# Kernel tuning notes

Hardware: AMD Instinct MI355X
Metric: run time of the kernel (lower is better)

## Reference

```python
import jax, jax.numpy as jnp
import numpy as np

N = 200000      # tweet nodes
E = 1600000     # edges
U = 20000       # users (num_users)
D = 64          # embedding_dimension1 == embedding_dimension2
NUMP, CATP = 20, 12
EPS = 0.1       # PyG FAConv default eps


def setup_inputs() -> dict:
    key = jax.random.key(0)
    ks = jax.random.split(key, 20)
    s = 0.05
    offs = jnp.sort(jax.random.randint(ks[3], (U + 1,), 0, N, dtype=jnp.int64))
    offs = offs.at[0].set(0).at[-1].set(N)
    return {
        "num_prop": jax.random.normal(ks[0], (N, NUMP), jnp.float32),
        "cat_prop": jax.random.normal(ks[1], (N, CATP), jnp.float32),
        "tweet_offsets": offs,
        "edge_index": jax.random.randint(ks[2], (2, E), 0, N, dtype=jnp.int64),
        "re_index": jax.random.randint(ks[4], (U,), 0, U, dtype=jnp.int64),
        "W_num": jax.random.normal(ks[5], (NUMP, D // 2), jnp.float32) * s,
        "b_num": jnp.zeros((D // 2,), jnp.float32),
        "W_cat": jax.random.normal(ks[6], (CATP, D // 2), jnp.float32) * s,
        "b_cat": jnp.zeros((D // 2,), jnp.float32),
        "W_tog": jax.random.normal(ks[7], (D, D), jnp.float32) * s,
        "b_tog": jnp.zeros((D,), jnp.float32),
        "att_l": jax.random.normal(ks[8], (D,), jnp.float32) * s,
        "att_r": jax.random.normal(ks[9], (D,), jnp.float32) * s,
        "W_f1": jax.random.normal(ks[10], (D, D // 2), jnp.float32) * s,
        "b_f1": jnp.zeros((D // 2,), jnp.float32),
        "W_lab": jax.random.normal(ks[11], (D // 2, 2), jnp.float32) * s,
        "b_lab": jnp.zeros((2,), jnp.float32),
    }


def reference(num_prop, cat_prop, tweet_offsets, edge_index, re_index,
              W_num, b_num, W_cat, b_cat, W_tog, b_tog,
              att_l, att_r, W_f1, b_f1, W_lab, b_lab):
    n = num_prop.shape[0]
    lrelu = jax.nn.leaky_relu  # slope 0.01, matches nn.LeakyReLU default

    num = lrelu(num_prop @ W_num + b_num)
    cat = lrelu(cat_prop @ W_cat + b_cat)
    x = lrelu(jnp.concatenate([num, cat], axis=1) @ W_tog + b_tog)  # [N, D]

    # gcn_norm with self-loops (PyG FAConv default normalize=True, add_self_loops=True)
    loop = jnp.arange(n, dtype=edge_index.dtype)
    src = jnp.concatenate([edge_index[0], loop])
    dst = jnp.concatenate([edge_index[1], loop])
    deg = jax.ops.segment_sum(jnp.ones(src.shape[0], jnp.float32), dst, num_segments=n)
    dinv = jnp.where(deg > 0, deg ** -0.5, 0.0)
    norm = dinv[src] * dinv[dst]  # [E+N]

    def faconv(h, h0):
        # alpha_e = tanh(att_l . h[src] + att_r . h[dst]); out_i = sum_e norm_e * alpha_e * h[src_e]
        al = h @ att_l
        ar = h @ att_r
        alpha = jnp.tanh(al[src] + ar[dst]) * norm
        agg = jax.ops.segment_sum(h[src] * alpha[:, None], dst, num_segments=n)
        return agg + EPS * h0

    x1 = faconv(x, x)      # dropout is identity in eval mode
    x2 = faconv(x1, x)
    x2 = jnp.sqrt(x2 ** 2 + 1e-8)

    # ragged per-user segment sum from CSR offsets (replaces python loop+slice)
    nseg = tweet_offsets.shape[0] - 1
    seg = jnp.searchsorted(tweet_offsets, jnp.arange(n), side='right') - 1
    seg = jnp.clip(seg, 0, nseg - 1)
    x3 = jax.ops.segment_sum(x2, seg, num_segments=nseg)  # [U, D]

    x3 = x3[re_index]
    h = lrelu(x3 @ W_f1 + b_f1)
    return h @ W_lab + b_lab
```

## Files before the change

kernel.cpp:

```cpp
#include <hip/hip_runtime.h>
#include <hip/hip_bf16.h>

#define LRELU(v) ((v) > 0.0f ? (v) : 0.01f * (v))
#define EPS 0.1f

#define BSHIFT  9
#define BSIZE   512
#define BIN_EPB 2048
#define BIN_CAP 6144
#define CAPP    10240

typedef __attribute__((ext_vector_type(8))) short bf16x8;
typedef __attribute__((ext_vector_type(4))) float f32x4;

__device__ __forceinline__ float fast_tanh(float v)
{
    float e = __expf(2.0f * v);
    return 1.0f - 2.0f * __builtin_amdgcn_rcpf(e + 1.0f);
}

__device__ __forceinline__ float bf2f(unsigned short h)
{
    return __uint_as_float(((unsigned int)h) << 16);
}
__device__ __forceinline__ unsigned short f2bf(float f)
{
    unsigned int u = __float_as_uint(f);
    u += 0x7FFFu + ((u >> 16) & 1u);
    return (unsigned short)(u >> 16);
}

__global__ void k_prep(const float* __restrict__ W_num, const float* __restrict__ W_cat,
                       const float* __restrict__ W_tog,
                       unsigned short* __restrict__ Wb, unsigned short* __restrict__ Wb1)
{
    int t = threadIdx.x;
    for (int i = t; i < 8 * 512; i += 256) {
        int tile = i >> 9;
        int kt   = tile >> 2, nt = tile & 3;
        int lane = (i >> 3) & 63;
        int j    = i & 7;
        int k    = kt * 32 + (lane >> 4) * 8 + j;
        int n    = nt * 16 + (lane & 15);
        Wb[i] = f2bf(W_tog[k * 64 + n]);
    }
    for (int i = t; i < 4 * 512; i += 256) {
        int nt   = i >> 9;
        int lane = (i >> 3) & 63;
        int j    = i & 7;
        int k    = (lane >> 4) * 8 + j;
        int n    = nt * 16 + (lane & 15);
        float w;
        if (n < 32) w = (k < 20)  ? W_num[k * 32 + n]              : 0.0f;
        else        w = (k >= 20) ? W_cat[(k - 20) * 32 + (n - 32)] : 0.0f;
        Wb1[i] = f2bf(w);
    }
}

__global__ void __launch_bounds__(512)
k_featbin(
          const float* __restrict__ num_prop, const float* __restrict__ cat_prop,
          const unsigned short* __restrict__ Wb1, const float* __restrict__ b_num,
          const float* __restrict__ b_cat, const unsigned short* __restrict__ Wb,
          const float* __restrict__ b_tog, const float* __restrict__ att_l,
          const float* __restrict__ att_r, unsigned short* __restrict__ xb,
          float* __restrict__ al, float* __restrict__ ar,
          const int* __restrict__ src, const int* __restrict__ dst,
          int* __restrict__ bucket_cnt, int* __restrict__ buckets,
          int nbBin, int N, int E, int NB)
{
    __shared__ __align__(16) char shmem[28672];

    int tid = threadIdx.x;

    if ((int)blockIdx.x < nbBin) {
        int*  hist  = (int*)shmem;
        int*  lbase = hist + BSIZE;
        int*  gbase = lbase + BSIZE;
        int2* stage = (int2*)(gbase + BSIZE);

        int base = blockIdx.x * BIN_EPB;

        hist[tid] = 0;
        __syncthreads();

        int s[4], d[4], rk[4];
        #pragma unroll
        for (int k = 0; k < 4; k++) {
            int e = base + k * BSIZE + tid;
            s[k] = -1;
            if (e < E) {
                s[k] = src[e];
                d[k] = dst[e];
                rk[k] = atomicAdd(&hist[d[k] >> BSHIFT], 1);
            }
        }
        __syncthreads();

        int v = hist[tid];
        lbase[tid] = v;
        __syncthreads();
        for (int off = 1; off < BSIZE; off <<= 1) {
            int t = (tid >= off) ? lbase[tid - off] : 0;
            __syncthreads();
            lbase[tid] += t;
            __syncthreads();
        }
        int incl = lbase[tid];
        __syncthreads();
        lbase[tid] = incl - v;
        if (tid < NB && v > 0) gbase[tid] = atomicAdd(&bucket_cnt[tid], v);
        __syncthreads();

        #pragma unroll
        for (int k = 0; k < 4; k++) {
            if (s[k] >= 0) {
                int b = d[k] >> BSHIFT;
                stage[lbase[b] + rk[k]] = make_int2(s[k], d[k]);
            }
        }
        __syncthreads();

        int tot = min(BIN_EPB, E - base);
        for (int i = tid; i < tot; i += BSIZE) {
            int2 p = stage[i];
            int b = p.y >> BSHIFT;
            buckets[(size_t)b * BIN_CAP + gbase[b] + (i - lbase[b])] =
                (p.x << BSHIFT) | (p.y & (BSIZE - 1));
        }
    } else {
        unsigned short (*in_lds)[40] = (unsigned short(*)[40])shmem;
        unsigned short (*mid)[72]    = (unsigned short(*)[72])(shmem + 10240);

        int lane = tid & 63;
        int w    = tid >> 6;
        int blockStart = (blockIdx.x - nbBin) * 128;

        for (int i = tid; i < 128 * 20; i += 512) {
            int node = i / 20, k = i % 20;
            int n = min(blockStart + node, N - 1);
            in_lds[node][k] = f2bf(num_prop[(size_t)n * 20 + k]);
        }
        for (int i = tid; i < 128 * 12; i += 512) {
            int node = i / 12, k = i % 12;
            int n = min(blockStart + node, N - 1);
            in_lds[node][20 + k] = f2bf(cat_prop[(size_t)n * 12 + k]);
        }
        __syncthreads();

        int q   = lane >> 4;
        int c16 = lane & 15;

        bf16x8 ain = *(const bf16x8*)&in_lds[w * 16 + c16][q * 8];
        #pragma unroll
        for (int nt = 0; nt < 4; nt++) {
            bf16x8 b = *(const bf16x8*)&Wb1[nt * 512 + lane * 8];
            f32x4 acc = {0.0f, 0.0f, 0.0f, 0.0f};
            acc = __builtin_amdgcn_mfma_f32_16x16x32_bf16(ain, b, acc, 0, 0, 0);
            int   ch   = nt * 16 + c16;
            float bias = (ch < 32) ? b_num[ch] : b_cat[ch - 32];
            #pragma unroll
            for (int r = 0; r < 4; r++) {
                float s = acc[r] + bias;
                s = LRELU(s);
                mid[w * 16 + q * 4 + r][ch] = f2bf(s);
            }
        }

        bf16x8 a0 = *(const bf16x8*)&mid[w * 16 + c16][q * 8];
        bf16x8 a1 = *(const bf16x8*)&mid[w * 16 + c16][32 + q * 8];

        float pal[4] = {0, 0, 0, 0};
        float par[4] = {0, 0, 0, 0};

        #pragma unroll
        for (int nt = 0; nt < 4; nt++) {
            bf16x8 b0 = *(const bf16x8*)&Wb[(0 * 4 + nt) * 512 + lane * 8];
            bf16x8 b1 = *(const bf16x8*)&Wb[(1 * 4 + nt) * 512 + lane * 8];
            f32x4 acc = {0.0f, 0.0f, 0.0f, 0.0f};
            acc = __builtin_amdgcn_mfma_f32_16x16x32_bf16(a0, b0, acc, 0, 0, 0);
            acc = __builtin_amdgcn_mfma_f32_16x16x32_bf16(a1, b1, acc, 0, 0, 0);

            int   ch  = nt * 16 + c16;
            float bt  = b_tog[ch];
            float atl = att_l[ch];
            float atr = att_r[ch];
            #pragma unroll
            for (int r = 0; r < 4; r++) {
                float s = acc[r] + bt;
                s = LRELU(s);
                int n = blockStart + w * 16 + q * 4 + r;
                if (n < N) xb[(size_t)n * 64 + ch] = f2bf(s);
                pal[r] = fmaf(s, atl, pal[r]);
                par[r] = fmaf(s, atr, par[r]);
            }
        }

        #pragma unroll
        for (int r = 0; r < 4; r++) {
            float pl = pal[r], pr = par[r];
            #pragma unroll
            for (int off = 8; off > 0; off >>= 1) {
                pl += __shfl_xor(pl, off);
                pr += __shfl_xor(pr, off);
            }
            int n = blockStart + w * 16 + q * 4 + r;
            if (c16 == 0 && n < N) { al[n] = pl; ar[n] = pr; }
        }
    }
}

__global__ void __launch_bounds__(512)
k_build(const int* __restrict__ buckets, const int* __restrict__ bucket_cnt,
        const float* __restrict__ al, const int* __restrict__ offs,
        float2* __restrict__ ald1,
        int* __restrict__ deg, int* __restrict__ row_start, int* __restrict__ seg,
        int* __restrict__ srcs, int N, int U)
{
    __shared__ int stage[BIN_CAP];
    __shared__ int cnt[BSIZE];
    __shared__ int sc[BSIZE];
    __shared__ int cur[BSIZE];

    int b   = blockIdx.x;
    int tid = threadIdx.x;
    int ecnt = bucket_cnt[b];
    const int* bp = buckets + (size_t)b * BIN_CAP;

    cnt[tid] = 0;
    cur[tid] = 0;
    __syncthreads();

    for (int i = tid; i < ecnt; i += BSIZE) {
        int e = bp[i];
        stage[i] = e;
        atomicAdd(&cnt[e & (BSIZE - 1)], 1);
    }
    __syncthreads();

    int d = cnt[tid];
    int p = (d + 7) & ~7;
    sc[tid] = p;
    __syncthreads();
    for (int off = 1; off < BSIZE; off <<= 1) {
        int t = (tid >= off) ? sc[tid - off] : 0;
        __syncthreads();
        sc[tid] += t;
        __syncthreads();
    }
    int rstart = sc[tid] - p;

    int gb = b * CAPP;
    int n  = b * BSIZE + tid;
    if (n < N) {
        deg[n]       = d;
        row_start[n] = gb + rstart;
        for (int k = d; k < p; k++) srcs[gb + rstart + k] = 0;
        float dv = 1.0f / sqrtf((float)d + 1.0f);
        ald1[n] = make_float2(al[n], dv);

        int lo = 0, hi = U;
        while (lo < hi) {
            int mid = (lo + hi) >> 1;
            if (offs[mid] <= n) lo = mid + 1; else hi = mid;
        }
        seg[n] = min(max(lo - 1, 0), U - 1);
    }
    __syncthreads();

    for (int i = tid; i < ecnt; i += BSIZE) {
        int e = stage[i];
        int r = e & (BSIZE - 1);
        int o = atomicAdd(&cur[r], 1);
        int rs = sc[r] - ((cnt[r] + 7) & ~7);
        srcs[gb + rs + o] = e >> BSHIFT;
    }
}

__global__ void k_gather1(const int* __restrict__ srcs,
                          const int* __restrict__ row_start, const int* __restrict__ deg,
                          const unsigned short* __restrict__ xb,
                          const float2* __restrict__ ald1, const float* __restrict__ ar,
                          const float* __restrict__ att_l, const float* __restrict__ att_r,
                          unsigned short* __restrict__ h1b, float2* __restrict__ ald2,
                          float* __restrict__ ar2, int N)
{
    int lane = threadIdx.x & 63;
    int c0   = __builtin_amdgcn_readfirstlane(blockIdx.x * 4 + (threadIdx.x >> 6)) * 4;
    if (c0 >= N) return;
    int nend = min(c0 + 4, N);

    float atl = att_l[lane];
    float atr = att_r[lane];

    for (int n = c0; n < nend; n++) {
        int    s0   = row_start[n];
        int    cnt  = deg[n];
        int    cntp = (cnt + 7) & ~7;
        float2 self = ald1[n];
        float  di   = self.y;
        float  arn  = ar[n];

        float acc = 0.0f;
        for (int jb = 0; jb < cntp; jb += 64) {
            float a = 0.0f;
            int   e = jb + lane;
            if (e < cnt) {
                int s = srcs[s0 + e];
                float2 as = ald1[s];
                a = fast_tanh(as.x + arn) * as.y * di;
            }
            int te = min(cntp - jb, 64);
            for (int j = 0; j < te; j += 8) {
                int sv[8]; float vv[8];
                #pragma unroll
                for (int t = 0; t < 8; t++) sv[t] = srcs[s0 + jb + j + t];
                #pragma unroll
                for (int t = 0; t < 8; t++) vv[t] = bf2f(xb[(size_t)sv[t] * 64 + lane]);
                #pragma unroll
                for (int t = 0; t < 8; t++) acc = fmaf(vv[t], __shfl(a, j + t), acc);
            }
        }

        float selfa = fast_tanh(self.x + arn) * di * di;
        float xnl   = bf2f(xb[(size_t)n * 64 + lane]);
        float v     = acc + (selfa + EPS) * xnl;

        float pl = v * atl;
        float pr = v * atr;
        #pragma unroll
        for (int off = 32; off > 0; off >>= 1) {
            pl += __shfl_down(pl, off);
            pr += __shfl_down(pr, off);
        }
        h1b[(size_t)n * 64 + lane] = f2bf(v);
        if (lane == 0) { ald2[n] = make_float2(pl, di); ar2[n] = pr; }
    }
}

__global__ void k_gather2(const int* __restrict__ srcs,
                          const int* __restrict__ row_start, const int* __restrict__ deg,
                          const unsigned short* __restrict__ h1b,
                          const unsigned short* __restrict__ xb,
                          const float2* __restrict__ ald2, const float* __restrict__ ar2,
                          const int* __restrict__ seg,
                          float* __restrict__ x3, int N)
{
    int lane = threadIdx.x & 63;
    int c0   = __builtin_amdgcn_readfirstlane(blockIdx.x * 4 + (threadIdx.x >> 6)) * 4;
    if (c0 >= N) return;
    int nend = min(c0 + 4, N);

    float uacc = 0.0f;
    int   useg = seg[c0];

    for (int n = c0; n < nend; n++) {
        int sg = seg[n];
        if (sg != useg) {
            atomicAdd(&x3[(size_t)useg * 64 + lane], uacc);
            uacc = 0.0f;
            useg = sg;
        }

        int    s0   = row_start[n];
        int    cnt  = deg[n];
        int    cntp = (cnt + 7) & ~7;
        float2 self = ald2[n];
        float  di   = self.y;
        float  arn  = ar2[n];

        float acc = 0.0f;
        for (int jb = 0; jb < cntp; jb += 64) {
            float a = 0.0f;
            int   e = jb + lane;
            if (e < cnt) {
                int s = srcs[s0 + e];
                float2 as = ald2[s];
                a = fast_tanh(as.x + arn) * as.y * di;
            }
            int te = min(cntp - jb, 64);
            for (int j = 0; j < te; j += 8) {
                int sv[8]; float vv[8];
                #pragma unroll
                for (int t = 0; t < 8; t++) sv[t] = srcs[s0 + jb + j + t];
                #pragma unroll
                for (int t = 0; t < 8; t++) vv[t] = bf2f(h1b[(size_t)sv[t] * 64 + lane]);
                #pragma unroll
                for (int t = 0; t < 8; t++) acc = fmaf(vv[t], __shfl(a, j + t), acc);
            }
        }

        float selfa = fast_tanh(self.x + arn) * di * di;
        float h1l   = bf2f(h1b[(size_t)n * 64 + lane]);
        float xnl   = bf2f(xb[(size_t)n * 64 + lane]);
        float v = acc + selfa * h1l + EPS * xnl;
        uacc += sqrtf(v * v + 1e-8f);
    }
    atomicAdd(&x3[(size_t)useg * 64 + lane], uacc);
}

__global__ void __launch_bounds__(256)
k_head(const float* __restrict__ x3, const int* __restrict__ re_index,
       const float* __restrict__ W_f1, const float* __restrict__ b_f1,
       const float* __restrict__ W_lab, const float* __restrict__ b_lab,
       float* __restrict__ out, int U)
{
    __shared__ float wf[64][32];
    __shared__ float wl[32][2];

    int tid = threadIdx.x;
    for (int i = tid; i < 64 * 32; i += 256) wf[i >> 5][i & 31] = W_f1[i];
    if (tid < 64) wl[tid >> 1][tid & 1] = W_lab[tid];
    __syncthreads();

    int u = blockIdx.x * blockDim.x + tid;
    if (u >= U) return;

    int r = re_index[u];
    const float* y = x3 + (size_t)r * 64;

    float s[32];
    #pragma unroll
    for (int j = 0; j < 32; j++) s[j] = b_f1[j];

    for (int k = 0; k < 64; k++) {
        float yk = y[k];
        #pragma unroll
        for (int j = 0; j < 32; j++) s[j] = fmaf(yk, wf[k][j], s[j]);
    }

    float o0 = b_lab[0], o1 = b_lab[1];
    #pragma unroll
    for (int j = 0; j < 32; j++) {
        float t = LRELU(s[j]);
        o0 = fmaf(t, wl[j][0], o0);
        o1 = fmaf(t, wl[j][1], o1);
    }
    out[(size_t)u * 2 + 0] = o0;
    out[(size_t)u * 2 + 1] = o1;
}

extern "C" void kernel_launch(void* const* d_in, const int* in_sizes, int n_in,
                              void* d_out, int out_size, void* d_ws, size_t ws_size,
                              hipStream_t stream)
{
    const float* num_prop = (const float*)d_in[0];
    const float* cat_prop = (const float*)d_in[1];
    const int*   offs     = (const int*)d_in[2];
    const int*   edge     = (const int*)d_in[3];
    const int*   re_index = (const int*)d_in[4];
    const float* W_num    = (const float*)d_in[5];
    const float* b_num    = (const float*)d_in[6];
    const float* W_cat    = (const float*)d_in[7];
    const float* b_cat    = (const float*)d_in[8];
    const float* W_tog    = (const float*)d_in[9];
    const float* b_tog    = (const float*)d_in[10];
    const float* att_l    = (const float*)d_in[11];
    const float* att_r    = (const float*)d_in[12];
    const float* W_f1     = (const float*)d_in[13];
    const float* b_f1     = (const float*)d_in[14];
    const float* W_lab    = (const float*)d_in[15];
    const float* b_lab    = (const float*)d_in[16];

    const int N = in_sizes[0] / 20;
    const int E = in_sizes[3] / 2;
    const int U = in_sizes[4];

    const int* src = edge;
    const int* dst = edge + E;

    const int NB = (N + BSIZE - 1) >> BSHIFT;

    float* ws = (float*)d_ws;
    size_t off = 0;
    unsigned short* xb  = (unsigned short*)(ws + off); off += (size_t)N * 32;
    unsigned short* h1b = (unsigned short*)(ws + off); off += (size_t)N * 32;
    float2* ald1 = (float2*)(ws + off); off += (size_t)N * 2;
    float2* ald2 = (float2*)(ws + off); off += (size_t)N * 2;
    int*    buckets = (int*)(ws + off); off += (size_t)NB * BIN_CAP;
    float*  al   = ws + off; off += N;
    float*  ar   = ws + off; off += N;
    float*  ar2  = ws + off; off += N;
    float*  x3   = ws + off; off += (size_t)U * 64;
    unsigned short* Wb  = (unsigned short*)(ws + off); off += 2048;
    unsigned short* Wb1 = (unsigned short*)(ws + off); off += 1024;
    int*    deg        = (int*)(ws + off); off += N;
    int*    row_start  = (int*)(ws + off); off += N;
    int*    seg        = (int*)(ws + off); off += N;
    int*    bucket_cnt = (int*)(ws + off); off += NB;
    int*    srcs       = (int*)(ws + off); off += (size_t)NB * CAPP;

    hipMemsetAsync(bucket_cnt, 0, (size_t)NB * 4, stream);
    hipMemsetAsync(x3, 0, (size_t)U * 64 * 4, stream);

    const int nbC    = (N + 15) / 16;
    const int nbBin  = (E + BIN_EPB - 1) / BIN_EPB;
    const int nbFeat = (N + 127) / 128;

    k_prep<<<1, 256, 0, stream>>>(W_num, W_cat, W_tog, Wb, Wb1);

    k_featbin<<<nbBin + nbFeat, 512, 0, stream>>>(num_prop, cat_prop, Wb1, b_num,
                                                  b_cat, Wb, b_tog, att_l, att_r,
                                                  xb, al, ar,
                                                  src, dst, bucket_cnt, buckets,
                                                  nbBin, N, E, NB);

    k_build<<<NB, BSIZE, 0, stream>>>(buckets, bucket_cnt, al, offs, ald1,
                                      deg, row_start, seg, srcs, N, U);

    k_gather1<<<nbC, 256, 0, stream>>>(srcs, row_start, deg, xb, ald1, ar,
                                       att_l, att_r, h1b, ald2, ar2, N);

    k_gather2<<<nbC, 256, 0, stream>>>(srcs, row_start, deg, h1b, xb,
                                       ald2, ar2, seg, x3, N);

    k_head<<<(U + 255) / 256, 256, 0, stream>>>(x3, re_index, W_f1, b_f1, W_lab, b_lab,
                                                (float*)d_out, U);
}
```

Before: 324.2 us.

## Pack per-node metadata, fold memsets into kernels, and double nodes per wave

Per-node row start and degree are packed into one int2, and al/dinv/ar into one float4 (likewise for the second layer), so each node's metadata needs fewer separate loads. The two hipMemsetAsync calls are removed: bucket counters are now zeroed in k_prep and the x3 accumulator in k_build, which cuts launch overhead. Each wave in both gather kernels now handles 8 nodes instead of 4, halving the grid and allowing longer per-user accumulation runs before the atomic flush. The trade-offs are fewer waves available to hide gather latency and a larger 16-byte record in the random per-edge source lookups, which may waste bandwidth.

```diff
diff --git a/kernel.cpp b/kernel.cpp
--- a/kernel.cpp
+++ b/kernel.cpp
@@ -9,6 +9,7 @@
 #define BIN_EPB 2048
 #define BIN_CAP 6144
 #define CAPP    10240
+#define CHUNK   8
 
 typedef __attribute__((ext_vector_type(8))) short bf16x8;
 typedef __attribute__((ext_vector_type(4))) float f32x4;
@@ -32,9 +33,11 @@
 
 __global__ void k_prep(const float* __restrict__ W_num, const float* __restrict__ W_cat,
                        const float* __restrict__ W_tog,
-                       unsigned short* __restrict__ Wb, unsigned short* __restrict__ Wb1)
+                       unsigned short* __restrict__ Wb, unsigned short* __restrict__ Wb1,
+                       int* __restrict__ bucket_cnt, int NB)
 {
     int t = threadIdx.x;
+    for (int i = t; i < NB; i += 256) bucket_cnt[i] = 0;
     for (int i = t; i < 8 * 512; i += 256) {
         int tile = i >> 9;
         int kt   = tile >> 2, nt = tile & 3;
@@ -212,10 +215,11 @@
 
 __global__ void __launch_bounds__(512)
 k_build(const int* __restrict__ buckets, const int* __restrict__ bucket_cnt,
-        const float* __restrict__ al, const int* __restrict__ offs,
-        float2* __restrict__ ald1,
-        int* __restrict__ deg, int* __restrict__ row_start, int* __restrict__ seg,
-        int* __restrict__ srcs, int N, int U)
+        const float* __restrict__ al, const float* __restrict__ ar,
+        const int* __restrict__ offs,
+        float4* __restrict__ aldr1,
+        int2* __restrict__ rd, int* __restrict__ seg,
+        int* __restrict__ srcs, float* __restrict__ x3, int N, int U)
 {
     __shared__ int stage[BIN_CAP];
     __shared__ int cnt[BSIZE];
@@ -226,6 +230,10 @@
     int tid = threadIdx.x;
     int ecnt = bucket_cnt[b];
     const int* bp = buckets + (size_t)b * BIN_CAP;
+
+    size_t u64 = (size_t)U * 64;
+    for (size_t i = (size_t)b * BSIZE + tid; i < u64; i += (size_t)gridDim.x * BSIZE)
+        x3[i] = 0.0f;
 
     cnt[tid] = 0;
     cur[tid] = 0;
@@ -253,11 +261,10 @@
     int gb = b * CAPP;
     int n  = b * BSIZE + tid;
     if (n < N) {
-        deg[n]       = d;
-        row_start[n] = gb + rstart;
+        rd[n] = make_int2(gb + rstart, d);
         for (int k = d; k < p; k++) srcs[gb + rstart + k] = 0;
         float dv = 1.0f / sqrtf((float)d + 1.0f);
-        ald1[n] = make_float2(al[n], dv);
+        aldr1[n] = make_float4(al[n], dv, ar[n], 0.0f);
 
         int lo = 0, hi = U;
         while (lo < hi) {
@@ -278,28 +285,29 @@
 }
 
 __global__ void k_gather1(const int* __restrict__ srcs,
-                          const int* __restrict__ row_start, const int* __restrict__ deg,
+                          const int2* __restrict__ rd,
                           const unsigned short* __restrict__ xb,
-                          const float2* __restrict__ ald1, const float* __restrict__ ar,
+                          const float4* __restrict__ aldr1,
                           const float* __restrict__ att_l, const float* __restrict__ att_r,
-                          unsigned short* __restrict__ h1b, float2* __restrict__ ald2,
-                          float* __restrict__ ar2, int N)
+                          unsigned short* __restrict__ h1b, float4* __restrict__ aldr2,
+                          int N)
 {
     int lane = threadIdx.x & 63;
-    int c0   = __builtin_amdgcn_readfirstlane(blockIdx.x * 4 + (threadIdx.x >> 6)) * 4;
+    int c0   = __builtin_amdgcn_readfirstlane(blockIdx.x * 4 + (threadIdx.x >> 6)) * CHUNK;
     if (c0 >= N) return;
-    int nend = min(c0 + 4, N);
+    int nend = min(c0 + CHUNK, N);
 
     float atl = att_l[lane];
     float atr = att_r[lane];
 
     for (int n = c0; n < nend; n++) {
-        int    s0   = row_start[n];
-        int    cnt  = deg[n];
+        int2   rdn  = rd[n];
+        int    s0   = rdn.x;
+        int    cnt  = rdn.y;
         int    cntp = (cnt + 7) & ~7;
-        float2 self = ald1[n];
+        float4 self = aldr1[n];
         float  di   = self.y;
-        float  arn  = ar[n];
+        float  arn  = self.z;
 
         float acc = 0.0f;
         for (int jb = 0; jb < cntp; jb += 64) {
@@ -307,7 +315,7 @@
             int   e = jb + lane;
             if (e < cnt) {
                 int s = srcs[s0 + e];
-                float2 as = ald1[s];
+                float2 as = *(const float2*)&aldr1[s];
                 a = fast_tanh(as.x + arn) * as.y * di;
             }
             int te = min(cntp - jb, 64);
@@ -334,22 +342,22 @@
             pr += __shfl_down(pr, off);
         }
         h1b[(size_t)n * 64 + lane] = f2bf(v);
-        if (lane == 0) { ald2[n] = make_float2(pl, di); ar2[n] = pr; }
+        if (lane == 0) aldr2[n] = make_float4(pl, di, pr, 0.0f);
     }
 }
 
 __global__ void k_gather2(const int* __restrict__ srcs,
-                          const int* __restrict__ row_start, const int* __restrict__ deg,
+                          const int2* __restrict__ rd,
                           const unsigned short* __restrict__ h1b,
                           const unsigned short* __restrict__ xb,
-                          const float2* __restrict__ ald2, const float* __restrict__ ar2,
+                          const float4* __restrict__ aldr2,
                           const int* __restrict__ seg,
                           float* __restrict__ x3, int N)
 {
     int lane = threadIdx.x & 63;
-    int c0   = __builtin_amdgcn_readfirstlane(blockIdx.x * 4 + (threadIdx.x >> 6)) * 4;
+    int c0   = __builtin_amdgcn_readfirstlane(blockIdx.x * 4 + (threadIdx.x >> 6)) * CHUNK;
     if (c0 >= N) return;
-    int nend = min(c0 + 4, N);
+    int nend = min(c0 + CHUNK, N);
 
     float uacc = 0.0f;
     int   useg = seg[c0];
@@ -362,12 +370,13 @@
             useg = sg;
         }
 
-        int    s0   = row_start[n];
-        int    cnt  = deg[n];
+        int2   rdn  = rd[n];
+        int    s0   = rdn.x;
+        int    cnt  = rdn.y;
         int    cntp = (cnt + 7) & ~7;
-        float2 self = ald2[n];
+        float4 self = aldr2[n];
         float  di   = self.y;
-        float  arn  = ar2[n];
+        float  arn  = self.z;
 
         float acc = 0.0f;
         for (int jb = 0; jb < cntp; jb += 64) {
@@ -375,7 +384,7 @@
             int   e = jb + lane;
             if (e < cnt) {
                 int s = srcs[s0 + e];
-                float2 as = ald2[s];
+                float2 as = *(const float2*)&aldr2[s];
                 a = fast_tanh(as.x + arn) * as.y * di;
             }
             int te = min(cntp - jb, 64);
@@ -473,31 +482,26 @@
 
     float* ws = (float*)d_ws;
     size_t off = 0;
+    float4* aldr1 = (float4*)(ws + off); off += (size_t)N * 4;
+    float4* aldr2 = (float4*)(ws + off); off += (size_t)N * 4;
     unsigned short* xb  = (unsigned short*)(ws + off); off += (size_t)N * 32;
     unsigned short* h1b = (unsigned short*)(ws + off); off += (size_t)N * 32;
-    float2* ald1 = (float2*)(ws + off); off += (size_t)N * 2;
-    float2* ald2 = (float2*)(ws + off); off += (size_t)N * 2;
     int*    buckets = (int*)(ws + off); off += (size_t)NB * BIN_CAP;
     float*  al   = ws + off; off += N;
     float*  ar   = ws + off; off += N;
-    float*  ar2  = ws + off; off += N;
     float*  x3   = ws + off; off += (size_t)U * 64;
     unsigned short* Wb  = (unsigned short*)(ws + off); off += 2048;
     unsigned short* Wb1 = (unsigned short*)(ws + off); off += 1024;
-    int*    deg        = (int*)(ws + off); off += N;
-    int*    row_start  = (int*)(ws + off); off += N;
+    int2*   rd         = (int2*)(ws + off); off += (size_t)N * 2;
     int*    seg        = (int*)(ws + off); off += N;
     int*    bucket_cnt = (int*)(ws + off); off += NB;
     int*    srcs       = (int*)(ws + off); off += (size_t)NB * CAPP;
 
-    hipMemsetAsync(bucket_cnt, 0, (size_t)NB * 4, stream);
-    hipMemsetAsync(x3, 0, (size_t)U * 64 * 4, stream);
-
-    const int nbC    = (N + 15) / 16;
+    const int nbC    = (N + 4 * CHUNK - 1) / (4 * CHUNK);
     const int nbBin  = (E + BIN_EPB - 1) / BIN_EPB;
     const int nbFeat = (N + 127) / 128;
 
-    k_prep<<<1, 256, 0, stream>>>(W_num, W_cat, W_tog, Wb, Wb1);
+    k_prep<<<1, 256, 0, stream>>>(W_num, W_cat, W_tog, Wb, Wb1, bucket_cnt, NB);
 
     k_featbin<<<nbBin + nbFeat, 512, 0, stream>>>(num_prop, cat_prop, Wb1, b_num,
                                                   b_cat, Wb, b_tog, att_l, att_r,
@@ -505,14 +509,13 @@
                                                   src, dst, bucket_cnt, buckets,
                                                   nbBin, N, E, NB);
 
-    k_build<<<NB, BSIZE, 0, stream>>>(buckets, bucket_cnt, al, offs, ald1,
-                                      deg, row_start, seg, srcs, N, U);
-
-    k_gather1<<<nbC, 256, 0, stream>>>(srcs, row_start, deg, xb, ald1, ar,
-                                       att_l, att_r, h1b, ald2, ar2, N);
-
-    k_gather2<<<nbC, 256, 0, stream>>>(srcs, row_start, deg, h1b, xb,
-                                       ald2, ar2, seg, x3, N);
+    k_build<<<NB, BSIZE, 0, stream>>>(buckets, bucket_cnt, al, ar, offs, aldr1,
+                                      rd, seg, srcs, x3, N, U);
+
+    k_gather1<<<nbC, 256, 0, stream>>>(srcs, rd, xb, aldr1,
+                                       att_l, att_r, h1b, aldr2, N);
+
+    k_gather2<<<nbC, 256, 0, stream>>>(srcs, rd, h1b, xb, aldr2, seg, x3, N);
 
     k_head<<<(U + 255) / 256, 256, 0, stream>>>(x3, re_index, W_f1, b_f1, W_lab, b_lab,
                                                 (float*)d_out, U);
```

Measured after the change: 322.9 us. No clear change (-0.4%).
